# Kernel optimization log

Hardware: AMD Instinct MI355X
Metric: run time of the kernel (lower is better)

## Reference

```python
import jax, jax.numpy as jnp
import numpy as np

N = 50000       # nodes
E = 800000      # edges (before self-loops)
IN_DIM = 8
H = 4           # heads (layers 1-2)
D = 32          # per-head hidden dim
HD = H * D      # 128
BN_EPS = 1e-5
NEG_SLOPE = 0.2


def _gat_conv(x, src, dst, W, a_src, a_dst, b, heads, concat):
    """PyG-style GATConv (eval mode, self-loops already in src/dst)."""
    n = x.shape[0]
    h = (x @ W).reshape(n, heads, -1)                      # [N, H, D]
    al_s = jnp.einsum('nhd,hd->nh', h, a_src)              # [N, H]
    al_d = jnp.einsum('nhd,hd->nh', h, a_dst)              # [N, H]
    e = jax.nn.leaky_relu(al_s[src] + al_d[dst], NEG_SLOPE)  # [E', H]
    m = jax.ops.segment_max(e, dst, num_segments=n)
    m = jnp.where(jnp.isfinite(m), m, 0.0)
    ex = jnp.exp(e - m[dst])
    den = jax.ops.segment_sum(ex, dst, num_segments=n)
    alpha = ex / (den[dst] + 1e-16)                        # [E', H] neighborhood softmax
    out = jax.ops.segment_sum(alpha[:, :, None] * h[src], dst, num_segments=n)  # [N, H, D]
    out = out.reshape(n, -1) if concat else out.mean(axis=1)
    return out + b


def _bn(x, g, b, m, v):
    return (x - m) * jax.lax.rsqrt(v + BN_EPS) * g + b


def setup_inputs() -> dict:
    key = jax.random.key(0)
    ks = jax.random.split(key, 32)
    f32 = jnp.float32
    d = {}
    d['x'] = jax.random.normal(ks[0], (N, IN_DIM), dtype=f32)
    d['edge_index'] = jax.random.randint(ks[1], (2, E), 0, N, dtype=jnp.int64)
    # layer 1: GAT(8 -> 32, 4 heads, concat)
    d['W1'] = jax.random.normal(ks[2], (IN_DIM, HD), dtype=f32) * 0.3
    d['as1'] = jax.random.normal(ks[3], (H, D), dtype=f32) * 0.3
    d['ad1'] = jax.random.normal(ks[4], (H, D), dtype=f32) * 0.3
    d['b1'] = jax.random.normal(ks[5], (HD,), dtype=f32) * 0.1
    d['g1'] = 1.0 + 0.1 * jax.random.normal(ks[6], (HD,), dtype=f32)
    d['be1'] = 0.1 * jax.random.normal(ks[7], (HD,), dtype=f32)
    d['m1'] = 0.1 * jax.random.normal(ks[8], (HD,), dtype=f32)
    d['v1'] = jax.random.uniform(ks[9], (HD,), dtype=f32, minval=0.5, maxval=1.5)
    # layer 2: GAT(128 -> 32, 4 heads, concat)
    d['W2'] = jax.random.normal(ks[10], (HD, HD), dtype=f32) * 0.1
    d['as2'] = jax.random.normal(ks[11], (H, D), dtype=f32) * 0.3
    d['ad2'] = jax.random.normal(ks[12], (H, D), dtype=f32) * 0.3
    d['b2'] = jax.random.normal(ks[13], (HD,), dtype=f32) * 0.1
    d['g2'] = 1.0 + 0.1 * jax.random.normal(ks[14], (HD,), dtype=f32)
    d['be2'] = 0.1 * jax.random.normal(ks[15], (HD,), dtype=f32)
    d['m2'] = 0.1 * jax.random.normal(ks[16], (HD,), dtype=f32)
    d['v2'] = jax.random.uniform(ks[17], (HD,), dtype=f32, minval=0.5, maxval=1.5)
    # layer 3: GAT(128 -> 32, 1 head, no concat)
    d['W3'] = jax.random.normal(ks[18], (HD, D), dtype=f32) * 0.1
    d['as3'] = jax.random.normal(ks[19], (1, D), dtype=f32) * 0.3
    d['ad3'] = jax.random.normal(ks[20], (1, D), dtype=f32) * 0.3
    d['b3'] = jax.random.normal(ks[21], (D,), dtype=f32) * 0.1
    d['g3'] = 1.0 + 0.1 * jax.random.normal(ks[22], (D,), dtype=f32)
    d['be3'] = 0.1 * jax.random.normal(ks[23], (D,), dtype=f32)
    d['m3'] = 0.1 * jax.random.normal(ks[24], (D,), dtype=f32)
    d['v3'] = jax.random.uniform(ks[25], (D,), dtype=f32, minval=0.5, maxval=1.5)
    # classifier: Linear(32->16) -> ReLU -> Linear(16->1)
    d['cW1'] = jax.random.normal(ks[26], (D, 16), dtype=f32) * 0.2
    d['cb1'] = 0.1 * jax.random.normal(ks[27], (16,), dtype=f32)
    d['cW2'] = jax.random.normal(ks[28], (16, 1), dtype=f32) * 0.2
    d['cb2'] = 0.1 * jax.random.normal(ks[29], (1,), dtype=f32)
    return d


def reference(x, edge_index, W1, as1, ad1, b1, g1, be1, m1, v1,
              W2, as2, ad2, b2, g2, be2, m2, v2,
              W3, as3, ad3, b3, g3, be3, m3, v3,
              cW1, cb1, cW2, cb2):
    n = x.shape[0]
    loop = jnp.arange(n, dtype=edge_index.dtype)
    src = jnp.concatenate([edge_index[0], loop])   # PyG adds self-loops
    dst = jnp.concatenate([edge_index[1], loop])
    x1 = jax.nn.elu(_bn(_gat_conv(x, src, dst, W1, as1, ad1, b1, H, True), g1, be1, m1, v1))
    x2 = jax.nn.elu(_bn(_gat_conv(x1, src, dst, W2, as2, ad2, b2, H, True), g2, be2, m2, v2))
    x3 = jax.nn.elu(_bn(_gat_conv(x2, src, dst, W3, as3, ad3, b3, 1, False), g3, be3, m3, v3))
    hidden = jax.nn.relu(x3 @ cW1 + cb1)
    return jax.nn.sigmoid(hidden @ cW2 + cb2)      # [N, 1]
```

## Files before the change

### kernel.cpp

```cpp
#include <hip/hip_runtime.h>
#include <hip/hip_bf16.h>

#define BN_EPS 1e-5f
#define CAPB 6144
#define LOG2E 1.4426950408889634f

typedef unsigned short ushort_t;
typedef __attribute__((ext_vector_type(2))) float f32x2;
typedef __attribute__((ext_vector_type(4))) float f32x4v;
typedef __attribute__((ext_vector_type(8))) short short8;

__device__ __forceinline__ float blo(unsigned w) { unsigned t = w << 16; return __builtin_bit_cast(float, t); }
__device__ __forceinline__ float bhi(unsigned w) { unsigned t = w & 0xffff0000u; return __builtin_bit_cast(float, t); }
__device__ __forceinline__ ushort_t bfbits(float a) {
  return (ushort_t)__builtin_bit_cast(unsigned short, __float2bfloat16(a));
}
__device__ __forceinline__ unsigned packbf2(float a, float b) {
  unsigned lo = (unsigned)bfbits(a);
  unsigned hi = (unsigned)bfbits(b);
  return lo | (hi << 16);
}
__device__ __forceinline__ float fexp2(float x) {
#if __has_builtin(__builtin_amdgcn_exp2f)
  return __builtin_amdgcn_exp2f(x);
#else
  return exp2f(x);
#endif
}
__device__ __forceinline__ void pkfma(f32x2& d, f32x2 a, f32x2 b) {
  asm("v_pk_fma_f32 %0, %1, %2, %0" : "+v"(d) : "v"(a), "v"(b));
}


__global__ __launch_bounds__(256) void k_binit(int* __restrict__ gCur, int nb) {
  int i = blockIdx.x * 256 + threadIdx.x;
  if (i < nb) gCur[i] = i * CAPB;
}

__global__ __launch_bounds__(256) void k_bucket(const int* __restrict__ ei, int E, int etot,
                                                unsigned* __restrict__ bkt, int* __restrict__ gCur,
                                                int nb) {
  __shared__ int sm[256];
  __shared__ int lstart[256];
  __shared__ int lcur[256];
  __shared__ int gbase[256];
  __shared__ unsigned stage[1024];
  int tid = threadIdx.x;
  int base = blockIdx.x * 1024;
  int cnt = etot - base; if (cnt > 1024) cnt = 1024;

  sm[tid] = 0;
  __syncthreads();
  unsigned key[4]; int have[4];
  #pragma unroll
  for (int u = 0; u < 4; ++u) {
    int idx = tid + u * 256;
    have[u] = (idx < cnt);
    if (have[u]) {
      int i = base + idx;
      int s, d;
      if (i < E) { s = ei[i]; d = ei[E + i]; }
      else       { s = i - E; d = s; }
      unsigned k = ((unsigned)d << 16) | (unsigned)s;
      key[u] = k;
      atomicAdd(&sm[k >> 24], 1);
    }
  }
  __syncthreads();
  int myc = sm[tid];
  #pragma unroll
  for (int off = 1; off < 256; off <<= 1) {
    int t = sm[tid];
    int u = (tid >= off) ? sm[tid - off] : 0;
    __syncthreads();
    sm[tid] = t + u;
    __syncthreads();
  }
  int excl = sm[tid] - myc;
  lstart[tid] = excl;
  lcur[tid] = excl;
  if (tid < nb) gbase[tid] = atomicAdd(&gCur[tid], myc);
  __syncthreads();
  #pragma unroll
  for (int u = 0; u < 4; ++u) {
    if (have[u]) {
      int bin = key[u] >> 24;
      int pos = atomicAdd(&lcur[bin], 1);
      stage[pos] = key[u];
    }
  }
  __syncthreads();
  for (int j = tid; j < cnt; j += 256) {
    unsigned k = stage[j];
    int bin = k >> 24;
    bkt[(size_t)gbase[bin] + (j - lstart[bin])] = k;
  }
}

__global__ __launch_bounds__(256) void k_csr(const unsigned* __restrict__ bkt,
                                             const int* __restrict__ gCur,
                                             int* __restrict__ csr, int* __restrict__ offs,
                                             int n, int nb, int etot) {
  __shared__ int sm[256];
  __shared__ int lstart[256];
  __shared__ int lcur[256];
  __shared__ unsigned itm[CAPB];
  __shared__ ushort_t limg[CAPB];
  int tid = threadIdx.x, b = blockIdx.x;
  int cnt = gCur[b] - b * CAPB;

  int c = 0;
  if (tid < nb) c = gCur[tid] - tid * CAPB;
  sm[tid] = c;
  __syncthreads();
  #pragma unroll
  for (int off = 1; off < 256; off <<= 1) {
    int t = sm[tid];
    int u = (tid >= off) ? sm[tid - off] : 0;
    __syncthreads();
    sm[tid] = t + u;
    __syncthreads();
  }
  int gbase = sm[b] - cnt;
  __syncthreads();

  sm[tid] = 0;
  __syncthreads();
  for (int j = tid; j < cnt; j += 256) {
    unsigned k = bkt[(size_t)b * CAPB + j];
    itm[j] = k;
    atomicAdd(&sm[(k >> 16) & 255], 1);
  }
  __syncthreads();
  int myc = sm[tid];
  #pragma unroll
  for (int off = 1; off < 256; off <<= 1) {
    int t = sm[tid];
    int u = (tid >= off) ? sm[tid - off] : 0;
    __syncthreads();
    sm[tid] = t + u;
    __syncthreads();
  }
  int excl = sm[tid] - myc;
  lstart[tid] = excl;
  lcur[tid] = excl;
  __syncthreads();
  for (int j = tid; j < cnt; j += 256) {
    unsigned k = itm[j];
    int d = (k >> 16) & 255;
    int pos = atomicAdd(&lcur[d], 1);
    limg[pos] = (ushort_t)(k & 0xffffu);
  }
  __syncthreads();
  for (int j = tid; j < cnt; j += 256) csr[gbase + j] = (int)limg[j];
  int gd = b * 256 + tid;
  if (gd < n) offs[gd] = gbase + lstart[tid];
  if (b == nb - 1 && tid == 0) offs[n] = etot;
}


__global__ __launch_bounds__(256) void k_wconv(const float* __restrict__ W2, const float* __restrict__ W3,
                                               ushort_t* __restrict__ Wt2, ushort_t* __restrict__ Wt3) {
  int t = blockIdx.x * 256 + threadIdx.x;
  const int np = 128 * 128;
  if (t < np) {
    int c = t / 128, k = t % 128;
    Wt2[t] = bfbits(W2[k * 128 + c]);
  } else if (t < np + 32 * 128) {
    int i = t - np;
    int c = i / 128, k = i % 128;
    Wt3[i] = bfbits(W3[k * 32 + c]);
  }
}


__global__ __launch_bounds__(256) void k_gemm1(const float* __restrict__ X,
    const float* __restrict__ W, const float* __restrict__ a_s, const float* __restrict__ a_d,
    ushort_t* __restrict__ Hout, float* __restrict__ als, float* __restrict__ ald, int n) {
  int wid = (blockIdx.x * 256 + threadIdx.x) >> 6;
  if (wid >= n) return;
  int lane = threadIdx.x & 63;
  int c0 = lane * 2;
  int h = lane >> 4;
  float4 xa = *(const float4*)&X[(size_t)wid * 8];
  float4 xb = *(const float4*)&X[(size_t)wid * 8 + 4];
  float x[8] = {xa.x, xa.y, xa.z, xa.w, xb.x, xb.y, xb.z, xb.w};
  float acc0 = 0.f, acc1 = 0.f;
  #pragma unroll
  for (int k = 0; k < 8; ++k) {
    float2 wv = *(const float2*)&W[k * 128 + c0];
    acc0 += x[k] * wv.x;
    acc1 += x[k] * wv.y;
  }
  *(unsigned*)&Hout[(size_t)wid * 128 + c0] = packbf2(acc0, acc1);
  int ci = c0 & 31;
  float ps = acc0 * a_s[h * 32 + ci] + acc1 * a_s[h * 32 + ci + 1];
  float pd = acc0 * a_d[h * 32 + ci] + acc1 * a_d[h * 32 + ci + 1];
  ps *= LOG2E; pd *= LOG2E;
  #pragma unroll
  for (int m = 1; m < 16; m <<= 1) {
    ps += __shfl_xor(ps, m, 64);
    pd += __shfl_xor(pd, m, 64);
  }
  if ((lane & 15) == 0) {
    als[(size_t)wid * 4 + h] = ps;
    ald[(size_t)wid * 4 + h] = pd;
  }
}


template<int FOUT>
__global__ __launch_bounds__(256) void k_gemm_mfma(
    const ushort_t* __restrict__ X, const ushort_t* __restrict__ Wt,
    const float* __restrict__ a_s, const float* __restrict__ a_d,
    ushort_t* __restrict__ Hout, float* __restrict__ als, float* __restrict__ ald, int n) {
  constexpr int HEADS = FOUT / 32;
  constexpr int MF = (FOUT == 128) ? 4 : 1;
  constexpr int BM = 64;
  constexpr int LDC = FOUT + 8;
  __shared__ ushort_t Ct[BM * LDC];
  int tid = threadIdx.x;
  int w = tid >> 6, lane = tid & 63;
  int lo = lane & 15, hi = lane >> 4;
  int rowB = blockIdx.x * BM;
  int row0 = (FOUT == 128) ? rowB : rowB + w * 16;
  int nbase = (FOUT == 128) ? w * 32 : 0;
  int h = (FOUT == 128) ? w : 0;

  f32x4v acc[MF][2];
  #pragma unroll
  for (int mf = 0; mf < MF; ++mf)
    #pragma unroll
    for (int nf = 0; nf < 2; ++nf) acc[mf][nf] = (f32x4v){0.f, 0.f, 0.f, 0.f};

  #pragma unroll
  for (int k0 = 0; k0 < 4; ++k0) {
    int kof = k0 * 32 + hi * 8;
    short8 b[2];
    #pragma unroll
    for (int nf = 0; nf < 2; ++nf) {
      int col = nbase + nf * 16 + lo;
      b[nf] = *(const short8*)&Wt[(size_t)col * 128 + kof];
    }
    short8 a[MF];
    #pragma unroll
    for (int mf = 0; mf < MF; ++mf) {
      int row = row0 + mf * 16 + lo;
      row = min(row, n - 1);
      a[mf] = *(const short8*)&X[(size_t)row * 128 + kof];
    }
    #pragma unroll
    for (int mf = 0; mf < MF; ++mf)
      #pragma unroll
      for (int nf = 0; nf < 2; ++nf)
        acc[mf][nf] = __builtin_amdgcn_mfma_f32_16x16x32_bf16(a[mf], b[nf], acc[mf][nf], 0, 0, 0);
  }

  float as0 = a_s[h * 32 + lo] * LOG2E, as1 = a_s[h * 32 + 16 + lo] * LOG2E;
  float ad0 = a_d[h * 32 + lo] * LOG2E, ad1 = a_d[h * 32 + 16 + lo] * LOG2E;
  #pragma unroll
  for (int mf = 0; mf < MF; ++mf) {
    #pragma unroll
    for (int j = 0; j < 4; ++j) {
      float ps = acc[mf][0][j] * as0 + acc[mf][1][j] * as1;
      float pd = acc[mf][0][j] * ad0 + acc[mf][1][j] * ad1;
      #pragma unroll
      for (int m = 1; m < 16; m <<= 1) {
        ps += __shfl_xor(ps, m, 64);
        pd += __shfl_xor(pd, m, 64);
      }
      if (lo == 0) {
        int row = row0 + mf * 16 + hi * 4 + j;
        if (row < n) {
          als[(size_t)row * HEADS + h] = ps;
          ald[(size_t)row * HEADS + h] = pd;
        }
      }
    }
  }

  #pragma unroll
  for (int mf = 0; mf < MF; ++mf) {
    int rL = ((FOUT == 128) ? 0 : w * 16) + mf * 16 + hi * 4;
    #pragma unroll
    for (int nf = 0; nf < 2; ++nf) {
      int cL = nbase + nf * 16 + lo;
      #pragma unroll
      for (int j = 0; j < 4; ++j)
        Ct[(rL + j) * LDC + cL] = bfbits(acc[mf][nf][j]);
    }
  }
  __syncthreads();
  constexpr int CPR = FOUT / 8;
  #pragma unroll
  for (int i = 0; i < (BM * CPR + 255) / 256; ++i) {
    int idx = tid + i * 256;
    if (idx < BM * CPR) {
      int r = idx / CPR, c = idx % CPR;
      int grow = rowB + r;
      if (grow < n)
        *(uint4*)&Hout[(size_t)grow * FOUT + c * 8] = *(const uint4*)&Ct[r * LDC + c * 8];
    }
  }
}


__device__ __forceinline__ int sel4(int eg, int a, int b, int c, int d) {
  int r = (eg & 1) ? b : a;
  int r2 = (eg & 1) ? d : c;
  return (eg & 2) ? r2 : r;
}

__global__ __launch_bounds__(256) void k_agg4(const int* __restrict__ offs, const int* __restrict__ csr,
    const ushort_t* __restrict__ Hb, const float* __restrict__ als, const float* __restrict__ ald,
    const float* __restrict__ bias, const float* __restrict__ gam, const float* __restrict__ bet,
    const float* __restrict__ mu, const float* __restrict__ var,
    ushort_t* __restrict__ Xo, int n) {
  constexpr int UB = 6;
  constexpr int CAPW = 120;
  __shared__ int   s_idx[4][CAPW];
  __shared__ float s_exp[4][CAPW * 4];
  int wslot = threadIdx.x >> 6;
  int wid = (blockIdx.x * 256 + threadIdx.x) >> 6;
  int v0 = wid * 4;
  if (v0 >= n) return;
  int lane = threadIdx.x & 63;

  int va = v0, vb = min(v0 + 1, n), vc = min(v0 + 2, n), vd = min(v0 + 3, n);
  int o0 = offs[va], o1 = offs[vb], o2 = offs[vc], o3 = offs[vd], o4 = offs[min(v0 + 4, n)];
  int d0 = o1 - o0, d1 = o2 - o1, d2 = o3 - o2, d3 = o4 - o3;

  int room = CAPW;
  int ms0 = min(d0, room); int mp0 = min((ms0 + UB - 1) / UB * UB, room); ms0 = min(ms0, mp0); room -= mp0;
  int ms1 = min(d1, room); int mp1 = min((ms1 + UB - 1) / UB * UB, room); ms1 = min(ms1, mp1); room -= mp1;
  int ms2 = min(d2, room); int mp2 = min((ms2 + UB - 1) / UB * UB, room); ms2 = min(ms2, mp2); room -= mp2;
  int ms3 = min(d3, room); int mp3 = min((ms3 + UB - 1) / UB * UB, room); ms3 = min(ms3, mp3);
  int p0 = 0, p1 = mp0, p2 = mp0 + mp1, p3 = mp0 + mp1 + mp2;

  int total = o4 - o0;
  for (int l = lane; l < total; l += 64) {
    int j = o0 + l;
    int nd = (j >= o1) + (j >= o2) + (j >= o3);
    int cbase = sel4(nd, o0 - p0, o1 - p1, o2 - p2, o3 - p3);
    int lim   = sel4(nd, p0 + ms0, p1 + ms1, p2 + ms2, p3 + ms3);
    int pos = j - cbase;
    if (pos < lim) {
      int s = csr[j];
      s_idx[wslot][pos] = s << 8;
      const float4 av = *(const float4*)&als[(size_t)s * 4];
      const float4 dv = *(const float4*)&ald[(size_t)(v0 + nd) * 4];
      float e0 = av.x + dv.x, e1 = av.y + dv.y, e2 = av.z + dv.z, e3 = av.w + dv.w;
      e0 = fmaxf(e0, 0.2f * e0); e1 = fmaxf(e1, 0.2f * e1);
      e2 = fmaxf(e2, 0.2f * e2); e3 = fmaxf(e3, 0.2f * e3);
      *(float4*)&s_exp[wslot][pos * 4] = make_float4(fexp2(e0), fexp2(e1), fexp2(e2), fexp2(e3));
    }
  }
  if (lane < 4 * UB) {
    int v = lane / UB, q = lane % UB;
    int msv = sel4(v, ms0, ms1, ms2, ms3);
    int mpv = sel4(v, mp0, mp1, mp2, mp3);
    int pv  = sel4(v, p0, p1, p2, p3);
    if (q < mpv - msv) {
      int pos = pv + msv + q;
      s_idx[wslot][pos] = 0;
      *(float4*)&s_exp[wslot][pos * 4] = make_float4(0.f, 0.f, 0.f, 0.f);
    }
  }

  int eg = lane >> 4;
  int fl = lane & 15;
  int f0 = fl * 8;
  int myh = f0 >> 5;
  int st  = sel4(eg, p0, p1, p2, p3);
  int mpv = sel4(eg, mp0, mp1, mp2, mp3);
  int msv = sel4(eg, ms0, ms1, ms2, ms3);
  int dgv = sel4(eg, d0, d1, d2, d3);
  int obv = sel4(eg, o0, o1, o2, o3);
  const char* hb = (const char*)Hb + f0 * 2;

  f32x2 acc2[4];
  #pragma unroll
  for (int q = 0; q < 4; ++q) acc2[q] = (f32x2){0.f, 0.f};
  float den = 0.f;

  for (int j0 = 0; j0 < mpv; j0 += UB) {
    int ss[UB]; float ex[UB];
    #pragma unroll
    for (int u = 0; u < UB; ++u) {
      int pidx = st + j0 + u;
      ss[u] = s_idx[wslot][pidx];
      ex[u] = s_exp[wslot][pidx * 4 + myh];
    }
    uint4 pv[UB];
    #pragma unroll
    for (int u = 0; u < UB; ++u)
      pv[u] = *(const uint4*)(hb + (size_t)(unsigned)ss[u]);
    #pragma unroll
    for (int u = 0; u < UB; ++u) {
      f32x2 e2v = (f32x2){ex[u], ex[u]};
      pkfma(acc2[0], e2v, (f32x2){blo(pv[u].x), bhi(pv[u].x)});
      pkfma(acc2[1], e2v, (f32x2){blo(pv[u].y), bhi(pv[u].y)});
      pkfma(acc2[2], e2v, (f32x2){blo(pv[u].z), bhi(pv[u].z)});
      pkfma(acc2[3], e2v, (f32x2){blo(pv[u].w), bhi(pv[u].w)});
    }
    den += ((ex[0] + ex[1]) + (ex[2] + ex[3])) + (ex[4] + ex[5]);
  }
  if (dgv > msv) {
    float myald = ald[(size_t)(v0 + eg) * 4 + myh];
    for (int j = msv; j < dgv; ++j) {
      int s = csr[obv + j];
      float e = als[(size_t)s * 4 + myh] + myald;
      e = fmaxf(e, 0.2f * e);
      float exv = fexp2(e);
      den += exv;
      uint4 pv = *(const uint4*)(Hb + (size_t)s * 128 + f0);
      f32x2 e2v = (f32x2){exv, exv};
      pkfma(acc2[0], e2v, (f32x2){blo(pv.x), bhi(pv.x)});
      pkfma(acc2[1], e2v, (f32x2){blo(pv.y), bhi(pv.y)});
      pkfma(acc2[2], e2v, (f32x2){blo(pv.z), bhi(pv.z)});
      pkfma(acc2[3], e2v, (f32x2){blo(pv.w), bhi(pv.w)});
    }
  }

  int node = v0 + eg;
  if (node >= n) return;
  float acc[8] = {acc2[0].x, acc2[0].y, acc2[1].x, acc2[1].y,
                  acc2[2].x, acc2[2].y, acc2[3].x, acc2[3].y};
  float inv = 1.f / (den + 1e-16f);
  float4 bi0 = *(const float4*)&bias[f0], bi1 = *(const float4*)&bias[f0 + 4];
  float4 mu0 = *(const float4*)&mu[f0],   mu1 = *(const float4*)&mu[f0 + 4];
  float4 va0 = *(const float4*)&var[f0],  va1 = *(const float4*)&var[f0 + 4];
  float4 ga0 = *(const float4*)&gam[f0],  ga1 = *(const float4*)&gam[f0 + 4];
  float4 be0 = *(const float4*)&bet[f0],  be1 = *(const float4*)&bet[f0 + 4];
  float bb[8] = {bi0.x, bi0.y, bi0.z, bi0.w, bi1.x, bi1.y, bi1.z, bi1.w};
  float mm[8] = {mu0.x, mu0.y, mu0.z, mu0.w, mu1.x, mu1.y, mu1.z, mu1.w};
  float vv[8] = {va0.x, va0.y, va0.z, va0.w, va1.x, va1.y, va1.z, va1.w};
  float gg[8] = {ga0.x, ga0.y, ga0.z, ga0.w, ga1.x, ga1.y, ga1.z, ga1.w};
  float ee[8] = {be0.x, be0.y, be0.z, be0.w, be1.x, be1.y, be1.z, be1.w};
  float ov[8];
  #pragma unroll
  for (int q = 0; q < 8; ++q) {
    float xo = acc[q] * inv + bb[q];
    xo = (xo - mm[q]) * rsqrtf(vv[q] + BN_EPS) * gg[q] + ee[q];
    ov[q] = (xo > 0.f) ? xo : (__expf(xo) - 1.f);
  }
  uint4 pk;
  pk.x = packbf2(ov[0], ov[1]); pk.y = packbf2(ov[2], ov[3]);
  pk.z = packbf2(ov[4], ov[5]); pk.w = packbf2(ov[6], ov[7]);
  *(uint4*)&Xo[(size_t)node * 128 + f0] = pk;
}


__global__ __launch_bounds__(256) void k_agg1(const int* __restrict__ offs, const int* __restrict__ csr,
    const ushort_t* __restrict__ Hb, const float* __restrict__ als, const float* __restrict__ ald,
    const float* __restrict__ bias, const float* __restrict__ gam, const float* __restrict__ bet,
    const float* __restrict__ mu, const float* __restrict__ var,
    float* __restrict__ Xo, int n) {
  constexpr int LPF = 4;
  constexpr int EPW = 16;
  constexpr int UB = 2;
  constexpr int STEP = 32;
  constexpr int CAP = 128;
  __shared__ int   s_idx[4][CAP];
  __shared__ float s_exp[4][CAP];
  int wslot = threadIdx.x >> 6;
  int wv = (blockIdx.x * 256 + threadIdx.x) >> 6;
  if (wv >= n) return;
  int lane = threadIdx.x & 63;
  int rs = offs[wv];
  int deg = offs[wv + 1] - rs;
  int dstage = deg < CAP ? deg : CAP;
  int dpad = ((dstage + STEP - 1) / STEP) * STEP;
  float ald0 = ald[wv];

  for (int j = lane; j < dpad; j += 64) {
    if (j < dstage) {
      int s = csr[rs + j];
      s_idx[wslot][j] = s << 6;
      float e = als[s] + ald0;
      e = fmaxf(e, 0.2f * e);
      s_exp[wslot][j] = fexp2(e);
    } else {
      s_idx[wslot][j] = 0;
      s_exp[wslot][j] = 0.f;
    }
  }

  int fl = lane % LPF;
  int eg = lane / LPF;
  int f0 = fl * 8;
  const char* hb = (const char*)Hb + f0 * 2;

  f32x2 acc2[4];
  #pragma unroll
  for (int q = 0; q < 4; ++q) acc2[q] = (f32x2){0.f, 0.f};
  float den = 0.f;

  for (int j0 = eg; j0 < dpad; j0 += STEP) {
    int ss[UB]; float ex[UB];
    #pragma unroll
    for (int u = 0; u < UB; ++u) {
      int j = j0 + u * EPW;
      ss[u] = s_idx[wslot][j];
      ex[u] = s_exp[wslot][j];
    }
    uint4 pv[UB];
    #pragma unroll
    for (int u = 0; u < UB; ++u)
      pv[u] = *(const uint4*)(hb + (size_t)(unsigned)ss[u]);
    #pragma unroll
    for (int u = 0; u < UB; ++u) {
      f32x2 e2v = (f32x2){ex[u], ex[u]};
      pkfma(acc2[0], e2v, (f32x2){blo(pv[u].x), bhi(pv[u].x)});
      pkfma(acc2[1], e2v, (f32x2){blo(pv[u].y), bhi(pv[u].y)});
      pkfma(acc2[2], e2v, (f32x2){blo(pv[u].z), bhi(pv[u].z)});
      pkfma(acc2[3], e2v, (f32x2){blo(pv[u].w), bhi(pv[u].w)});
      den += ex[u];
    }
  }
  if (deg > CAP) {
    for (int j = CAP + eg; j < deg; j += EPW) {
      int s = csr[rs + j];
      float e = als[s] + ald0;
      e = fmaxf(e, 0.2f * e);
      float exv = fexp2(e);
      den += exv;
      uint4 pv = *(const uint4*)(Hb + (size_t)s * 32 + f0);
      f32x2 e2v = (f32x2){exv, exv};
      pkfma(acc2[0], e2v, (f32x2){blo(pv.x), bhi(pv.x)});
      pkfma(acc2[1], e2v, (f32x2){blo(pv.y), bhi(pv.y)});
      pkfma(acc2[2], e2v, (f32x2){blo(pv.z), bhi(pv.z)});
      pkfma(acc2[3], e2v, (f32x2){blo(pv.w), bhi(pv.w)});
    }
  }

  float acc[8] = {acc2[0].x, acc2[0].y, acc2[1].x, acc2[1].y,
                  acc2[2].x, acc2[2].y, acc2[3].x, acc2[3].y};
  #pragma unroll
  for (int off = 32; off >= LPF; off >>= 1) {
    den += __shfl_xor(den, off, 64);
    #pragma unroll
    for (int q = 0; q < 8; ++q) acc[q] += __shfl_xor(acc[q], off, 64);
  }
  float inv = 1.f / (den + 1e-16f);

  if (lane < LPF) {
    float ov[8];
    #pragma unroll
    for (int q = 0; q < 8; ++q) {
      int f = f0 + q;
      float xo = acc[q] * inv + bias[f];
      xo = (xo - mu[f]) * rsqrtf(var[f] + BN_EPS) * gam[f] + bet[f];
      ov[q] = (xo > 0.f) ? xo : (__expf(xo) - 1.f);
    }
    *(float4*)(Xo + (size_t)wv * 32 + f0)     = make_float4(ov[0], ov[1], ov[2], ov[3]);
    *(float4*)(Xo + (size_t)wv * 32 + f0 + 4) = make_float4(ov[4], ov[5], ov[6], ov[7]);
  }
}


__global__ __launch_bounds__(256) void k_cls(const float* __restrict__ X3,
    const float* __restrict__ cW1, const float* __restrict__ cb1,
    const float* __restrict__ cW2, const float* __restrict__ cb2,
    float* __restrict__ out, int n) {
  int i = blockIdx.x * 256 + threadIdx.x;
  if (i >= n) return;
  float x[32];
  #pragma unroll
  for (int k = 0; k < 32; k += 4) {
    float4 v = *(const float4*)&X3[(size_t)i * 32 + k];
    x[k] = v.x; x[k + 1] = v.y; x[k + 2] = v.z; x[k + 3] = v.w;
  }
  float o = cb2[0];
  #pragma unroll
  for (int j = 0; j < 16; ++j) {
    float hs = cb1[j];
    #pragma unroll
    for (int k = 0; k < 32; ++k) hs += x[k] * cW1[k * 16 + j];
    hs = fmaxf(hs, 0.f);
    o += hs * cW2[j];
  }
  out[i] = 1.f / (1.f + __expf(-o));
}


static inline size_t align256(size_t x) { return (x + 255) & ~(size_t)255; }

extern "C" void kernel_launch(void* const* d_in, const int* in_sizes, int n_in,
                              void* d_out, int out_size, void* d_ws, size_t ws_size,
                              hipStream_t stream) {
  const float* x   = (const float*)d_in[0];
  const int*   ei  = (const int*)d_in[1];
  const float* W1  = (const float*)d_in[2];
  const float* as1 = (const float*)d_in[3];
  const float* ad1 = (const float*)d_in[4];
  const float* b1  = (const float*)d_in[5];
  const float* g1  = (const float*)d_in[6];
  const float* be1 = (const float*)d_in[7];
  const float* m1  = (const float*)d_in[8];
  const float* v1  = (const float*)d_in[9];
  const float* W2  = (const float*)d_in[10];
  const float* as2 = (const float*)d_in[11];
  const float* ad2 = (const float*)d_in[12];
  const float* b2  = (const float*)d_in[13];
  const float* g2  = (const float*)d_in[14];
  const float* be2 = (const float*)d_in[15];
  const float* m2  = (const float*)d_in[16];
  const float* v2  = (const float*)d_in[17];
  const float* W3  = (const float*)d_in[18];
  const float* as3 = (const float*)d_in[19];
  const float* ad3 = (const float*)d_in[20];
  const float* b3  = (const float*)d_in[21];
  const float* g3  = (const float*)d_in[22];
  const float* be3 = (const float*)d_in[23];
  const float* m3  = (const float*)d_in[24];
  const float* v3  = (const float*)d_in[25];
  const float* cW1 = (const float*)d_in[26];
  const float* cb1 = (const float*)d_in[27];
  const float* cW2 = (const float*)d_in[28];
  const float* cb2 = (const float*)d_in[29];

  const int n = in_sizes[0] / 8;
  const int E = in_sizes[1] / 2;
  const int etot = E + n;
  const int nb = (n + 255) / 256;

  char* p = (char*)d_ws;
  int* offs   = (int*)p;  p += align256((size_t)(n + 1) * 4);
  int* csr    = (int*)p;  p += align256((size_t)etot * 4);
  int* gCur   = (int*)p;  p += align256(1024);
  unsigned* bkt = (unsigned*)p; p += align256((size_t)nb * CAPB * 4);
  float* als  = (float*)p; p += align256((size_t)n * 4 * 4);
  float* ald  = (float*)p; p += align256((size_t)n * 4 * 4);
  ushort_t* bufH = (ushort_t*)p; p += align256((size_t)n * 128 * 2);
  ushort_t* bufX = (ushort_t*)p; p += align256((size_t)n * 128 * 2);
  float* x3f  = (float*)p; p += align256((size_t)n * 32 * 4);
  ushort_t* wt2 = (ushort_t*)p; p += align256(128 * 128 * 2);
  ushort_t* wt3 = (ushort_t*)p; p += align256(32 * 128 * 2);

  k_binit<<<(nb + 255) / 256, 256, 0, stream>>>(gCur, nb);
  k_bucket<<<(etot + 1023) / 1024, 256, 0, stream>>>(ei, E, etot, bkt, gCur, nb);
  k_csr<<<nb, 256, 0, stream>>>(bkt, gCur, csr, offs, n, nb, etot);
  k_wconv<<<80, 256, 0, stream>>>(W2, W3, wt2, wt3);

  const int ga4 = (n + 15) / 16;
  const int ga1 = (n + 3) / 4;

  k_gemm1<<<ga1, 256, 0, stream>>>(x, W1, as1, ad1, bufH, als, ald, n);
  k_agg4<<<ga4, 256, 0, stream>>>(offs, csr, bufH, als, ald, b1, g1, be1, m1, v1, bufX, n);

  k_gemm_mfma<128><<<(n + 63) / 64, 256, 0, stream>>>(bufX, wt2, as2, ad2, bufH, als, ald, n);
  k_agg4<<<ga4, 256, 0, stream>>>(offs, csr, bufH, als, ald, b2, g2, be2, m2, v2, bufX, n);

  k_gemm_mfma<32><<<(n + 63) / 64, 256, 0, stream>>>(bufX, wt3, as3, ad3, bufH, als, ald, n);
  k_agg1<<<ga1, 256, 0, stream>>>(offs, csr, bufH, als, ald, b3, g3, be3, m3, v3, x3f, n);

  k_cls<<<(n + 255) / 256, 256, 0, stream>>>(x3f, cW1, cb1, cW2, cb2, (float*)d_out, n);
}
```

Baseline: 198.8 us.

## Aggregate raw 8-dim inputs in layer 1 and apply W1 after aggregation

Layer 1 now precomputes the attention logit vectors W1·a_src/a_dst, so logits come straight from the 8-dim input in a small kernel. The aggregation gathers 8-float input rows instead of 128-wide bf16 hidden rows, and multiplies by W1 after the weighted sum, fused with bias, batchnorm and ELU. This reassociation uses linearity to cut gather bandwidth and removes the materialised layer-1 hidden tensor. The per-warp edge capacity in shared memory is also raised, and the 32-wide GEMM uses 256-row blocks with a simplified store loop.

```diff
diff --git a/kernel.cpp b/kernel.cpp
--- a/kernel.cpp
+++ b/kernel.cpp
@@ -159,8 +159,10 @@
 }
 
 
-__global__ __launch_bounds__(256) void k_wconv(const float* __restrict__ W2, const float* __restrict__ W3,
-                                               ushort_t* __restrict__ Wt2, ushort_t* __restrict__ Wt3) {
+__global__ __launch_bounds__(256) void k_wconv(
+    const float* __restrict__ W1, const float* __restrict__ as1, const float* __restrict__ ad1,
+    const float* __restrict__ W2, const float* __restrict__ W3,
+    ushort_t* __restrict__ Wt2, ushort_t* __restrict__ Wt3, float* __restrict__ wsd) {
   int t = blockIdx.x * 256 + threadIdx.x;
   const int np = 128 * 128;
   if (t < np) {
@@ -170,42 +172,194 @@
     int i = t - np;
     int c = i / 128, k = i % 128;
     Wt3[i] = bfbits(W3[k * 32 + c]);
-  }
-}
-
-
-__global__ __launch_bounds__(256) void k_gemm1(const float* __restrict__ X,
-    const float* __restrict__ W, const float* __restrict__ a_s, const float* __restrict__ a_d,
-    ushort_t* __restrict__ Hout, float* __restrict__ als, float* __restrict__ ald, int n) {
+  } else if (t < np + 32 * 128 + 64) {
+    int i = t - np - 32 * 128;
+    int h = (i >> 3) & 3, k = i & 7;
+    const float* av = (i & 32) ? ad1 : as1;
+    float acc = 0.f;
+    for (int c = 0; c < 32; ++c) acc += W1[k * 128 + h * 32 + c] * av[h * 32 + c];
+    wsd[i] = acc * LOG2E;
+  }
+}
+
+
+__global__ __launch_bounds__(256) void k_logit1(const float* __restrict__ X,
+    const float* __restrict__ wsd, float* __restrict__ als, float* __restrict__ ald, int n) {
+  int i = blockIdx.x * 256 + threadIdx.x;
+  if (i >= n) return;
+  float4 xa = *(const float4*)&X[(size_t)i * 8];
+  float4 xb = *(const float4*)&X[(size_t)i * 8 + 4];
+  float x[8] = {xa.x, xa.y, xa.z, xa.w, xb.x, xb.y, xb.z, xb.w};
+  float sv[4], dv[4];
+  #pragma unroll
+  for (int h = 0; h < 4; ++h) {
+    float s = 0.f, d = 0.f;
+    #pragma unroll
+    for (int k = 0; k < 8; ++k) {
+      s += x[k] * wsd[h * 8 + k];
+      d += x[k] * wsd[32 + h * 8 + k];
+    }
+    sv[h] = s; dv[h] = d;
+  }
+  *(float4*)&als[(size_t)i * 4] = make_float4(sv[0], sv[1], sv[2], sv[3]);
+  *(float4*)&ald[(size_t)i * 4] = make_float4(dv[0], dv[1], dv[2], dv[3]);
+}
+
+
+__device__ __forceinline__ int sel4(int eg, int a, int b, int c, int d) {
+  int r = (eg & 1) ? b : a;
+  int r2 = (eg & 1) ? d : c;
+  return (eg & 2) ? r2 : r;
+}
+
+
+__global__ __launch_bounds__(256) void k_agg4x(const int* __restrict__ offs, const int* __restrict__ csr,
+    const float* __restrict__ X, const float* __restrict__ als, const float* __restrict__ ald,
+    const float* __restrict__ W1,
+    const float* __restrict__ bias, const float* __restrict__ gam, const float* __restrict__ bet,
+    const float* __restrict__ mu, const float* __restrict__ var,
+    ushort_t* __restrict__ Xo, int n) {
+  constexpr int UB = 6;
+  constexpr int CAPW = 252;
+  __shared__ int   s_idx[4][CAPW];
+  __shared__ float s_exp[4][CAPW * 4];
+  __shared__ float aggL[4][4][4][8];
+  int wslot = threadIdx.x >> 6;
   int wid = (blockIdx.x * 256 + threadIdx.x) >> 6;
-  if (wid >= n) return;
+  int v0 = wid * 4;
+  if (v0 >= n) return;
   int lane = threadIdx.x & 63;
-  int c0 = lane * 2;
-  int h = lane >> 4;
-  float4 xa = *(const float4*)&X[(size_t)wid * 8];
-  float4 xb = *(const float4*)&X[(size_t)wid * 8 + 4];
-  float x[8] = {xa.x, xa.y, xa.z, xa.w, xb.x, xb.y, xb.z, xb.w};
-  float acc0 = 0.f, acc1 = 0.f;
+
+  int va = v0, vb = min(v0 + 1, n), vc = min(v0 + 2, n), vd = min(v0 + 3, n);
+  int o0 = offs[va], o1 = offs[vb], o2 = offs[vc], o3 = offs[vd], o4 = offs[min(v0 + 4, n)];
+  int d0 = o1 - o0, d1 = o2 - o1, d2 = o3 - o2, d3 = o4 - o3;
+
+  int room = CAPW;
+  int ms0 = min(d0, room); int mp0 = min((ms0 + UB - 1) / UB * UB, room); ms0 = min(ms0, mp0); room -= mp0;
+  int ms1 = min(d1, room); int mp1 = min((ms1 + UB - 1) / UB * UB, room); ms1 = min(ms1, mp1); room -= mp1;
+  int ms2 = min(d2, room); int mp2 = min((ms2 + UB - 1) / UB * UB, room); ms2 = min(ms2, mp2); room -= mp2;
+  int ms3 = min(d3, room); int mp3 = min((ms3 + UB - 1) / UB * UB, room); ms3 = min(ms3, mp3);
+  int p0 = 0, p1 = mp0, p2 = mp0 + mp1, p3 = mp0 + mp1 + mp2;
+
+  int total = o4 - o0;
+  for (int l = lane; l < total; l += 64) {
+    int j = o0 + l;
+    int nd = (j >= o1) + (j >= o2) + (j >= o3);
+    int cbase = sel4(nd, o0 - p0, o1 - p1, o2 - p2, o3 - p3);
+    int lim   = sel4(nd, p0 + ms0, p1 + ms1, p2 + ms2, p3 + ms3);
+    int pos = j - cbase;
+    if (pos < lim) {
+      int s = csr[j];
+      s_idx[wslot][pos] = s << 5;
+      const float4 av = *(const float4*)&als[(size_t)s * 4];
+      const float4 dv = *(const float4*)&ald[(size_t)(v0 + nd) * 4];
+      float e0 = av.x + dv.x, e1 = av.y + dv.y, e2 = av.z + dv.z, e3 = av.w + dv.w;
+      e0 = fmaxf(e0, 0.2f * e0); e1 = fmaxf(e1, 0.2f * e1);
+      e2 = fmaxf(e2, 0.2f * e2); e3 = fmaxf(e3, 0.2f * e3);
+      *(float4*)&s_exp[wslot][pos * 4] = make_float4(fexp2(e0), fexp2(e1), fexp2(e2), fexp2(e3));
+    }
+  }
+  if (lane < 4 * UB) {
+    int v = lane / UB, q = lane % UB;
+    int msv = sel4(v, ms0, ms1, ms2, ms3);
+    int mpv = sel4(v, mp0, mp1, mp2, mp3);
+    int pv  = sel4(v, p0, p1, p2, p3);
+    if (q < mpv - msv) {
+      int pos = pv + msv + q;
+      s_idx[wslot][pos] = 0;
+      *(float4*)&s_exp[wslot][pos * 4] = make_float4(0.f, 0.f, 0.f, 0.f);
+    }
+  }
+
+  int eg = lane >> 4;
+  int fl = lane & 15;
+  int myh = fl >> 2;
+  int kp = fl & 3;
+  int st  = sel4(eg, p0, p1, p2, p3);
+  int mpv = sel4(eg, mp0, mp1, mp2, mp3);
+  int msv = sel4(eg, ms0, ms1, ms2, ms3);
+  int dgv = sel4(eg, d0, d1, d2, d3);
+  int obv = sel4(eg, o0, o1, o2, o3);
+  const char* xb = (const char*)X + kp * 8;
+
+  f32x2 accx = (f32x2){0.f, 0.f};
+  float den = 0.f;
+
+  for (int j0 = 0; j0 < mpv; j0 += UB) {
+    int ss[UB]; float ex[UB];
+    #pragma unroll
+    for (int u = 0; u < UB; ++u) {
+      int pidx = st + j0 + u;
+      ss[u] = s_idx[wslot][pidx];
+      ex[u] = s_exp[wslot][pidx * 4 + myh];
+    }
+    f32x2 xv[UB];
+    #pragma unroll
+    for (int u = 0; u < UB; ++u)
+      xv[u] = *(const f32x2*)(xb + (size_t)(unsigned)ss[u]);
+    #pragma unroll
+    for (int u = 0; u < UB; ++u)
+      pkfma(accx, (f32x2){ex[u], ex[u]}, xv[u]);
+    den += ((ex[0] + ex[1]) + (ex[2] + ex[3])) + (ex[4] + ex[5]);
+  }
+  if (dgv > msv) {
+    float myald = ald[(size_t)(v0 + eg) * 4 + myh];
+    for (int j = msv; j < dgv; ++j) {
+      int s = csr[obv + j];
+      float e = als[(size_t)s * 4 + myh] + myald;
+      e = fmaxf(e, 0.2f * e);
+      float exv = fexp2(e);
+      den += exv;
+      f32x2 xv = *(const f32x2*)(xb + ((size_t)s << 5));
+      pkfma(accx, (f32x2){exv, exv}, xv);
+    }
+  }
+
+  aggL[wslot][eg][myh][kp * 2]     = accx.x;
+  aggL[wslot][eg][myh][kp * 2 + 1] = accx.y;
+
+  int node = v0 + eg;
+  if (node >= n) return;
+  float inv = 1.f / (den + 1e-16f);
+  float ax[8];
+  *(float4*)&ax[0] = *(const float4*)&aggL[wslot][eg][myh][0];
+  *(float4*)&ax[4] = *(const float4*)&aggL[wslot][eg][myh][4];
+
+  int f0 = fl * 8;
+  float acc[8];
+  #pragma unroll
+  for (int q = 0; q < 8; ++q) acc[q] = 0.f;
   #pragma unroll
   for (int k = 0; k < 8; ++k) {
-    float2 wv = *(const float2*)&W[k * 128 + c0];
-    acc0 += x[k] * wv.x;
-    acc1 += x[k] * wv.y;
-  }
-  *(unsigned*)&Hout[(size_t)wid * 128 + c0] = packbf2(acc0, acc1);
-  int ci = c0 & 31;
-  float ps = acc0 * a_s[h * 32 + ci] + acc1 * a_s[h * 32 + ci + 1];
-  float pd = acc0 * a_d[h * 32 + ci] + acc1 * a_d[h * 32 + ci + 1];
-  ps *= LOG2E; pd *= LOG2E;
-  #pragma unroll
-  for (int m = 1; m < 16; m <<= 1) {
-    ps += __shfl_xor(ps, m, 64);
-    pd += __shfl_xor(pd, m, 64);
-  }
-  if ((lane & 15) == 0) {
-    als[(size_t)wid * 4 + h] = ps;
-    ald[(size_t)wid * 4 + h] = pd;
-  }
+    float4 w0 = *(const float4*)&W1[k * 128 + f0];
+    float4 w1 = *(const float4*)&W1[k * 128 + f0 + 4];
+    acc[0] += ax[k] * w0.x; acc[1] += ax[k] * w0.y;
+    acc[2] += ax[k] * w0.z; acc[3] += ax[k] * w0.w;
+    acc[4] += ax[k] * w1.x; acc[5] += ax[k] * w1.y;
+    acc[6] += ax[k] * w1.z; acc[7] += ax[k] * w1.w;
+  }
+
+  float4 bi0 = *(const float4*)&bias[f0], bi1 = *(const float4*)&bias[f0 + 4];
+  float4 mu0 = *(const float4*)&mu[f0],   mu1 = *(const float4*)&mu[f0 + 4];
+  float4 va0 = *(const float4*)&var[f0],  va1 = *(const float4*)&var[f0 + 4];
+  float4 ga0 = *(const float4*)&gam[f0],  ga1 = *(const float4*)&gam[f0 + 4];
+  float4 be0 = *(const float4*)&bet[f0],  be1 = *(const float4*)&bet[f0 + 4];
+  float bb[8] = {bi0.x, bi0.y, bi0.z, bi0.w, bi1.x, bi1.y, bi1.z, bi1.w};
+  float mm[8] = {mu0.x, mu0.y, mu0.z, mu0.w, mu1.x, mu1.y, mu1.z, mu1.w};
+  float vv[8] = {va0.x, va0.y, va0.z, va0.w, va1.x, va1.y, va1.z, va1.w};
+  float gg[8] = {ga0.x, ga0.y, ga0.z, ga0.w, ga1.x, ga1.y, ga1.z, ga1.w};
+  float ee[8] = {be0.x, be0.y, be0.z, be0.w, be1.x, be1.y, be1.z, be1.w};
+  float ov[8];
+  #pragma unroll
+  for (int q = 0; q < 8; ++q) {
+    float xo = acc[q] * inv + bb[q];
+    xo = (xo - mm[q]) * rsqrtf(vv[q] + BN_EPS) * gg[q] + ee[q];
+    ov[q] = (xo > 0.f) ? xo : (__expf(xo) - 1.f);
+  }
+  uint4 pk;
+  pk.x = packbf2(ov[0], ov[1]); pk.y = packbf2(ov[2], ov[3]);
+  pk.z = packbf2(ov[4], ov[5]); pk.w = packbf2(ov[6], ov[7]);
+  *(uint4*)&Xo[(size_t)node * 128 + f0] = pk;
 }
 
 
@@ -215,21 +369,20 @@
     const float* __restrict__ a_s, const float* __restrict__ a_d,
     ushort_t* __restrict__ Hout, float* __restrict__ als, float* __restrict__ ald, int n) {
   constexpr int HEADS = FOUT / 32;
-  constexpr int MF = (FOUT == 128) ? 4 : 1;
-  constexpr int BM = 64;
+  constexpr int BM = (FOUT == 128) ? 64 : 256;
   constexpr int LDC = FOUT + 8;
   __shared__ ushort_t Ct[BM * LDC];
   int tid = threadIdx.x;
   int w = tid >> 6, lane = tid & 63;
   int lo = lane & 15, hi = lane >> 4;
   int rowB = blockIdx.x * BM;
-  int row0 = (FOUT == 128) ? rowB : rowB + w * 16;
+  int row0 = (FOUT == 128) ? rowB : rowB + w * 64;
   int nbase = (FOUT == 128) ? w * 32 : 0;
   int h = (FOUT == 128) ? w : 0;
 
-  f32x4v acc[MF][2];
-  #pragma unroll
-  for (int mf = 0; mf < MF; ++mf)
+  f32x4v acc[4][2];
+  #pragma unroll
+  for (int mf = 0; mf < 4; ++mf)
     #pragma unroll
     for (int nf = 0; nf < 2; ++nf) acc[mf][nf] = (f32x4v){0.f, 0.f, 0.f, 0.f};
 
@@ -242,15 +395,15 @@
       int col = nbase + nf * 16 + lo;
       b[nf] = *(const short8*)&Wt[(size_t)col * 128 + kof];
     }
-    short8 a[MF];
-    #pragma unroll
-    for (int mf = 0; mf < MF; ++mf) {
+    short8 a[4];
+    #pragma unroll
+    for (int mf = 0; mf < 4; ++mf) {
       int row = row0 + mf * 16 + lo;
       row = min(row, n - 1);
       a[mf] = *(const short8*)&X[(size_t)row * 128 + kof];
     }
     #pragma unroll
-    for (int mf = 0; mf < MF; ++mf)
+    for (int mf = 0; mf < 4; ++mf)
       #pragma unroll
       for (int nf = 0; nf < 2; ++nf)
         acc[mf][nf] = __builtin_amdgcn_mfma_f32_16x16x32_bf16(a[mf], b[nf], acc[mf][nf], 0, 0, 0);
@@ -259,7 +412,7 @@
   float as0 = a_s[h * 32 + lo] * LOG2E, as1 = a_s[h * 32 + 16 + lo] * LOG2E;
   float ad0 = a_d[h * 32 + lo] * LOG2E, ad1 = a_d[h * 32 + 16 + lo] * LOG2E;
   #pragma unroll
-  for (int mf = 0; mf < MF; ++mf) {
+  for (int mf = 0; mf < 4; ++mf) {
     #pragma unroll
     for (int j = 0; j < 4; ++j) {
       float ps = acc[mf][0][j] * as0 + acc[mf][1][j] * as1;
@@ -280,8 +433,8 @@
   }
 
   #pragma unroll
-  for (int mf = 0; mf < MF; ++mf) {
-    int rL = ((FOUT == 128) ? 0 : w * 16) + mf * 16 + hi * 4;
+  for (int mf = 0; mf < 4; ++mf) {
+    int rL = ((FOUT == 128) ? 0 : w * 64) + mf * 16 + hi * 4;
     #pragma unroll
     for (int nf = 0; nf < 2; ++nf) {
       int cL = nbase + nf * 16 + lo;
@@ -293,23 +446,15 @@
   __syncthreads();
   constexpr int CPR = FOUT / 8;
   #pragma unroll
-  for (int i = 0; i < (BM * CPR + 255) / 256; ++i) {
+  for (int i = 0; i < (BM * CPR) / 256; ++i) {
     int idx = tid + i * 256;
-    if (idx < BM * CPR) {
-      int r = idx / CPR, c = idx % CPR;
-      int grow = rowB + r;
-      if (grow < n)
-        *(uint4*)&Hout[(size_t)grow * FOUT + c * 8] = *(const uint4*)&Ct[r * LDC + c * 8];
-    }
-  }
-}
-
-
-__device__ __forceinline__ int sel4(int eg, int a, int b, int c, int d) {
-  int r = (eg & 1) ? b : a;
-  int r2 = (eg & 1) ? d : c;
-  return (eg & 2) ? r2 : r;
-}
+    int r = idx / CPR, c = idx % CPR;
+    int grow = rowB + r;
+    if (grow < n)
+      *(uint4*)&Hout[(size_t)grow * FOUT + c * 8] = *(const uint4*)&Ct[r * LDC + c * 8];
+  }
+}
+
 
 __global__ __launch_bounds__(256) void k_agg4(const int* __restrict__ offs, const int* __restrict__ csr,
     const ushort_t* __restrict__ Hb, const float* __restrict__ als, const float* __restrict__ ald,
@@ -317,7 +462,7 @@
     const float* __restrict__ mu, const float* __restrict__ var,
     ushort_t* __restrict__ Xo, int n) {
   constexpr int UB = 6;
-  constexpr int CAPW = 120;
+  constexpr int CAPW = 252;
   __shared__ int   s_idx[4][CAPW];
   __shared__ float s_exp[4][CAPW * 4];
   int wslot = threadIdx.x >> 6;
@@ -637,22 +782,23 @@
   float* x3f  = (float*)p; p += align256((size_t)n * 32 * 4);
   ushort_t* wt2 = (ushort_t*)p; p += align256(128 * 128 * 2);
   ushort_t* wt3 = (ushort_t*)p; p += align256(32 * 128 * 2);
+  float* wsd  = (float*)p; p += align256(64 * 4);
 
   k_binit<<<(nb + 255) / 256, 256, 0, stream>>>(gCur, nb);
   k_bucket<<<(etot + 1023) / 1024, 256, 0, stream>>>(ei, E, etot, bkt, gCur, nb);
   k_csr<<<nb, 256, 0, stream>>>(bkt, gCur, csr, offs, n, nb, etot);
-  k_wconv<<<80, 256, 0, stream>>>(W2, W3, wt2, wt3);
+  k_wconv<<<81, 256, 0, stream>>>(W1, as1, ad1, W2, W3, wt2, wt3, wsd);
 
   const int ga4 = (n + 15) / 16;
   const int ga1 = (n + 3) / 4;
 
-  k_gemm1<<<ga1, 256, 0, stream>>>(x, W1, as1, ad1, bufH, als, ald, n);
-  k_agg4<<<ga4, 256, 0, stream>>>(offs, csr, bufH, als, ald, b1, g1, be1, m1, v1, bufX, n);
+  k_logit1<<<(n + 255) / 256, 256, 0, stream>>>(x, wsd, als, ald, n);
+  k_agg4x<<<ga4, 256, 0, stream>>>(offs, csr, x, als, ald, W1, b1, g1, be1, m1, v1, bufX, n);
 
   k_gemm_mfma<128><<<(n + 63) / 64, 256, 0, stream>>>(bufX, wt2, as2, ad2, bufH, als, ald, n);
   k_agg4<<<ga4, 256, 0, stream>>>(offs, csr, bufH, als, ald, b2, g2, be2, m2, v2, bufX, n);
 
-  k_gemm_mfma<32><<<(n + 63) / 64, 256, 0, stream>>>(bufX, wt3, as3, ad3, bufH, als, ald, n);
+  k_gemm_mfma<32><<<(n + 255) / 256, 256, 0, stream>>>(bufX, wt3, as3, ad3, bufH, als, ald, n);
   k_agg1<<<ga1, 256, 0, stream>>>(offs, csr, bufH, als, ald, b3, g3, be3, m3, v3, x3f, n);
 
   k_cls<<<(n + 255) / 256, 256, 0, stream>>>(x3f, cW1, cb1, cW2, cb2, (float*)d_out, n);
```

Result: faster. 169.0 us (-15.0%).
